# Optimization experiments

Measured on AMD Instinct MI355X. Metric: run time of the kernel, lower is better.

## Reference

```python
import jax, jax.numpy as jnp
import numpy as np

N_NODES = 50000
N_EDGES = 800000
D = 128
L = 3


def setup_inputs() -> dict:
    key = jax.random.key(0)
    k1, k2, k3 = jax.random.split(key, 3)
    x = jax.random.normal(k1, (N_NODES, D), dtype=jnp.float32)
    edge_index = jax.random.randint(k2, (2, N_EDGES), 0, N_NODES, dtype=jnp.int64)
    # per-layer GCNConv weights [L, in, out], bias [L, out] (zeros, as nn.Linear default bias is small),
    # PReLU per-channel slopes initialized to 0.25 (torch default)
    Ws = jax.random.normal(k3, (L, D, D), dtype=jnp.float32) / np.sqrt(D)
    bs = jnp.zeros((L, D), dtype=jnp.float32)
    alphas = jnp.full((L, D), 0.25, dtype=jnp.float32)
    return {"x": x, "edge_index": edge_index, "Ws": Ws, "bs": bs, "alphas": alphas}


def reference(x, edge_index, Ws, bs, alphas):
    N = x.shape[0]
    # PyG gcn_norm with edge_weight=None: unit weights, add self-loops (fill value 1),
    # symmetric normalization deg^{-1/2}[row] * deg^{-1/2}[col], aggregate at col (target).
    loop = jnp.arange(N, dtype=edge_index.dtype)
    row = jnp.concatenate([edge_index[0], loop])  # [E+N] source
    col = jnp.concatenate([edge_index[1], loop])  # [E+N] target
    deg = jax.ops.segment_sum(jnp.ones(row.shape[0], x.dtype), col, num_segments=N)
    dinv = jax.lax.rsqrt(deg)  # deg >= 1 due to self-loops
    norm = dinv[row] * dinv[col]  # [E+N]

    z = x
    for l in range(Ws.shape[0]):
        h = z @ Ws[l]  # linear transform [N, D]
        # gather -> scale -> scatter-add aggregation
        agg = jax.ops.segment_sum(h[row] * norm[:, None], col, num_segments=N)
        out = agg + bs[l]
        z = jnp.where(out >= 0, out, alphas[l] * out)  # per-channel PReLU
    return z
```

## Files before the change

### kernel.cpp

```cpp
#include <hip/hip_runtime.h>

#define N_NODES 50000
#define N_EDGES 800000
#define D 128
#define L 3
#define CAP 56

typedef __attribute__((ext_vector_type(8))) short short8;
typedef __attribute__((ext_vector_type(16))) float f32x16;

__device__ __forceinline__ unsigned int bf16_rne(float f) {
  unsigned int u = __float_as_uint(f);
  return (u + 0x7FFFu + ((u >> 16) & 1u)) >> 16;
}


__global__ __launch_bounds__(256) void zero_k(unsigned int* deg) {
  int i = blockIdx.x * 256 + threadIdx.x;
  if (i < N_NODES) deg[i] = 0u;
}

__global__ __launch_bounds__(256) void build_k(const int* __restrict__ rows,
                                               const int* __restrict__ cols,
                                               unsigned int* deg,
                                               unsigned int* __restrict__ csr) {
  int e = blockIdx.x * 256 + threadIdx.x;
  if (e >= N_EDGES) return;
  int c = cols[e];
  unsigned int r = atomicAdd(&deg[c], 1u);
  if (r < CAP) csr[(size_t)c * CAP + r] = (unsigned int)rows[e];
}

__global__ __launch_bounds__(256) void dinv_k(float* dinv_f, const unsigned int* deg) {
  int i = blockIdx.x * 256 + threadIdx.x;
  if (i < N_NODES) dinv_f[i] = rsqrtf((float)(deg[i] + 1u));
}

__global__ __launch_bounds__(256) void wconv_k(const float* __restrict__ Ws,
                                               unsigned int* __restrict__ Whi,
                                               unsigned int* __restrict__ Wlo) {
  int id = blockIdx.x * 256 + threadIdx.x;
  if (id >= L * 128 * 64) return;
  int kd = id & 63;
  int c = (id >> 6) & 127;
  int l = id >> 13;
  const float* W = Ws + (size_t)l * D * D;
  float w0 = W[(size_t)(2 * kd) * 128 + c];
  float w1 = W[(size_t)(2 * kd + 1) * 128 + c];
  unsigned int h0 = bf16_rne(w0), h1 = bf16_rne(w1);
  float f0 = __uint_as_float(h0 << 16), f1 = __uint_as_float(h1 << 16);
  unsigned int l0 = bf16_rne(w0 - f0), l1 = bf16_rne(w1 - f1);
  Whi[id] = h0 | (h1 << 16);
  Wlo[id] = l0 | (l1 << 16);
}

__global__ __launch_bounds__(256) void gather_k(const unsigned int* __restrict__ deg,
                                                const unsigned int* __restrict__ csr,
                                                const float* __restrict__ dinv,
                                                const float* __restrict__ Z,
                                                unsigned int* __restrict__ AGGhi,
                                                unsigned int* __restrict__ AGGlo) {
  int wid = (blockIdx.x * 256 + threadIdx.x) >> 6;
  int lane = threadIdx.x & 63;
  if (wid >= N_NODES) return;
  const float2* Z2 = (const float2*)Z;
  float di = dinv[wid];
  float2 z = Z2[(size_t)wid * 64 + lane];
  float sx = di * z.x, sy = di * z.y;
  unsigned int cnt = deg[wid];
  if (cnt > CAP) cnt = CAP;
  unsigned int s = 0u;
  float w = 0.f;
  if (lane < (int)cnt) {
    s = csr[(size_t)wid * CAP + lane];
    w = dinv[s];
  }
  unsigned int j = 0;
  for (; j + 8u <= cnt; j += 8u) {
    unsigned int ss[8];
    float wws[8];
#pragma unroll
    for (int t = 0; t < 8; ++t) {
      ss[t] = __shfl(s, (int)(j + t), 64);
      wws[t] = __shfl(w, (int)(j + t), 64);
    }
    float2 v[8];
#pragma unroll
    for (int t = 0; t < 8; ++t) v[t] = Z2[(size_t)ss[t] * 64 + lane];
#pragma unroll
    for (int t = 0; t < 8; ++t) {
      sx += wws[t] * v[t].x;
      sy += wws[t] * v[t].y;
    }
  }
  for (; j < cnt; ++j) {
    unsigned int s0 = __shfl(s, (int)j, 64);
    float w0 = __shfl(w, (int)j, 64);
    float2 v0 = Z2[(size_t)s0 * 64 + lane];
    sx += w0 * v0.x;
    sy += w0 * v0.y;
  }
  sx *= di;
  sy *= di;
  unsigned int hx = bf16_rne(sx), hy = bf16_rne(sy);
  float fx = __uint_as_float(hx << 16), fy = __uint_as_float(hy << 16);
  unsigned int lx = bf16_rne(sx - fx), ly = bf16_rne(sy - fy);
  AGGhi[(size_t)wid * 64 + lane] = hx | (hy << 16);
  AGGlo[(size_t)wid * 64 + lane] = lx | (ly << 16);
}

__global__ __launch_bounds__(64) void gemm_mfma_k(const unsigned int* __restrict__ Phi,
                                                  const unsigned int* __restrict__ Plo,
                                                  const unsigned int* __restrict__ Whi,
                                                  const unsigned int* __restrict__ Wlo,
                                                  const float* __restrict__ bias,
                                                  const float* __restrict__ alpha,
                                                  float* __restrict__ out) {
  const int lane = threadIdx.x;
  const int kg = lane >> 5;
  const int cl = lane & 31;
  const int rb = blockIdx.x * 32;
  const int row = rb + cl;
  const int ar = row < N_NODES ? row : N_NODES - 1;

  f32x16 acc[4];
#pragma unroll
  for (int cf = 0; cf < 4; ++cf)
#pragma unroll
    for (int j = 0; j < 16; ++j) acc[cf][j] = 0.f;

#pragma unroll
  for (int ks = 0; ks < 8; ++ks) {
    int pb = ks * 8 + kg * 4;
    short8 ahi = *(const short8*)&Phi[(size_t)ar * 64 + pb];
    short8 alo = *(const short8*)&Plo[(size_t)ar * 64 + pb];
#pragma unroll
    for (int cf = 0; cf < 4; ++cf) {
      int cc = cf * 32 + cl;
      short8 bhi = *(const short8*)&Whi[(size_t)cc * 64 + pb];
      short8 blo = *(const short8*)&Wlo[(size_t)cc * 64 + pb];
      acc[cf] = __builtin_amdgcn_mfma_f32_32x32x16_bf16(ahi, bhi, acc[cf], 0, 0, 0);
      acc[cf] = __builtin_amdgcn_mfma_f32_32x32x16_bf16(ahi, blo, acc[cf], 0, 0, 0);
      acc[cf] = __builtin_amdgcn_mfma_f32_32x32x16_bf16(alo, bhi, acc[cf], 0, 0, 0);
    }
  }

#pragma unroll
  for (int cf = 0; cf < 4; ++cf) {
    int col = cf * 32 + cl;
    float bl = bias[col], al = alpha[col];
#pragma unroll
    for (int j = 0; j < 16; ++j) {
      int r = rb + 4 * kg + (j & 3) + 8 * (j >> 2);
      if (r < N_NODES) {
        float v = acc[cf][j] + bl;
        out[(size_t)r * D + col] = v >= 0.f ? v : al * v;
      }
    }
  }
}


extern "C" void kernel_launch(void* const* d_in, const int* in_sizes, int n_in,
                              void* d_out, int out_size, void* d_ws, size_t ws_size,
                              hipStream_t stream) {
  const float* x      = (const float*)d_in[0];
  const int*   ei     = (const int*)d_in[1];
  const float* Ws     = (const float*)d_in[2];
  const float* bs     = (const float*)d_in[3];
  const float* alphas = (const float*)d_in[4];
  float* out = (float*)d_out;

  const int* rows = ei;
  const int* cols = ei + N_EDGES;

  char* ws = (char*)d_ws;
  const size_t NPAD = (((size_t)N_NODES * 4 + 255) / 256) * 256;
  const size_t CSRPAD = (((size_t)N_NODES * CAP * 4 + 255) / 256) * 256;
  const size_t AGGPAD = (((size_t)N_NODES * 64 * 4 + 255) / 256) * 256;
  const size_t WPAD = (((size_t)L * 128 * 64 * 4 + 255) / 256) * 256;
  float*        dinv  = (float*)ws;         ws += NPAD;
  unsigned int* deg   = (unsigned int*)ws;  ws += NPAD;
  unsigned int* csr   = (unsigned int*)ws;  ws += CSRPAD;
  unsigned int* AGGhi = (unsigned int*)ws;  ws += AGGPAD;
  unsigned int* AGGlo = (unsigned int*)ws;  ws += AGGPAD;
  unsigned int* Whi   = (unsigned int*)ws;  ws += WPAD;
  unsigned int* Wlo   = (unsigned int*)ws;  ws += WPAD;
  float* Z = out;

  zero_k<<<(N_NODES + 255) / 256, 256, 0, stream>>>(deg);
  build_k<<<(N_EDGES + 255) / 256, 256, 0, stream>>>(rows, cols, deg, csr);
  dinv_k<<<(N_NODES + 255) / 256, 256, 0, stream>>>(dinv, deg);
  wconv_k<<<(L * 128 * 64 + 255) / 256, 256, 0, stream>>>(Ws, Whi, Wlo);

  for (int l = 0; l < L; ++l) {
    const float* zin = (l == 0) ? x : Z;
    gather_k<<<(N_NODES * 64 + 255) / 256, 256, 0, stream>>>(deg, csr, dinv, zin, AGGhi, AGGlo);
    gemm_mfma_k<<<(N_NODES + 31) / 32, 64, 0, stream>>>(
        AGGhi, AGGlo, Whi + (size_t)l * 128 * 64, Wlo + (size_t)l * 128 * 64,
        bs + (size_t)l * D, alphas + (size_t)l * D, Z);
  }
}
```

Before: 318.2 us.

## Stage weights in LDS for 4-wave GEMM blocks and fold dinv into gather

The GEMM kernel now uses 256-thread blocks covering 128 rows. Each block stages the hi/lo bf16 weight halves into padded shared memory, in two K-halves, so all four waves share them instead of each wave reading W from global or L2. Separately, the dinv kernel and its buffer are removed, and the gather kernel computes rsqrt(deg+1) inline for the node and its neighbors. This saves one launch, at the cost of extra rsqrt work and deg lookups during gather.

```diff
diff --git a/kernel.cpp b/kernel.cpp
--- a/kernel.cpp
+++ b/kernel.cpp
@@ -29,11 +29,6 @@
   int c = cols[e];
   unsigned int r = atomicAdd(&deg[c], 1u);
   if (r < CAP) csr[(size_t)c * CAP + r] = (unsigned int)rows[e];
-}
-
-__global__ __launch_bounds__(256) void dinv_k(float* dinv_f, const unsigned int* deg) {
-  int i = blockIdx.x * 256 + threadIdx.x;
-  if (i < N_NODES) dinv_f[i] = rsqrtf((float)(deg[i] + 1u));
 }
 
 __global__ __launch_bounds__(256) void wconv_k(const float* __restrict__ Ws,
@@ -56,7 +51,6 @@
 
 __global__ __launch_bounds__(256) void gather_k(const unsigned int* __restrict__ deg,
                                                 const unsigned int* __restrict__ csr,
-                                                const float* __restrict__ dinv,
                                                 const float* __restrict__ Z,
                                                 unsigned int* __restrict__ AGGhi,
                                                 unsigned int* __restrict__ AGGlo) {
@@ -64,16 +58,16 @@
   int lane = threadIdx.x & 63;
   if (wid >= N_NODES) return;
   const float2* Z2 = (const float2*)Z;
-  float di = dinv[wid];
+  unsigned int dg = deg[wid];
+  float di = rsqrtf((float)(dg + 1u));
   float2 z = Z2[(size_t)wid * 64 + lane];
   float sx = di * z.x, sy = di * z.y;
-  unsigned int cnt = deg[wid];
-  if (cnt > CAP) cnt = CAP;
+  unsigned int cnt = dg > CAP ? CAP : dg;
   unsigned int s = 0u;
   float w = 0.f;
   if (lane < (int)cnt) {
     s = csr[(size_t)wid * CAP + lane];
-    w = dinv[s];
+    w = rsqrtf((float)(deg[s] + 1u));
   }
   unsigned int j = 0;
   for (; j + 8u <= cnt; j += 8u) {
@@ -109,18 +103,22 @@
   AGGlo[(size_t)wid * 64 + lane] = lx | (ly << 16);
 }
 
-__global__ __launch_bounds__(64) void gemm_mfma_k(const unsigned int* __restrict__ Phi,
-                                                  const unsigned int* __restrict__ Plo,
-                                                  const unsigned int* __restrict__ Whi,
-                                                  const unsigned int* __restrict__ Wlo,
-                                                  const float* __restrict__ bias,
-                                                  const float* __restrict__ alpha,
-                                                  float* __restrict__ out) {
-  const int lane = threadIdx.x;
+__global__ __launch_bounds__(256) void gemm_mfma_k(const unsigned int* __restrict__ Phi,
+                                                   const unsigned int* __restrict__ Plo,
+                                                   const unsigned int* __restrict__ Whi,
+                                                   const unsigned int* __restrict__ Wlo,
+                                                   const float* __restrict__ bias,
+                                                   const float* __restrict__ alpha,
+                                                   float* __restrict__ out) {
+  __shared__ unsigned int sWhi[128 * 36];
+  __shared__ unsigned int sWlo[128 * 36];
+  const int tid = threadIdx.x;
+  const int lane = tid & 63;
+  const int w = tid >> 6;
   const int kg = lane >> 5;
   const int cl = lane & 31;
-  const int rb = blockIdx.x * 32;
-  const int row = rb + cl;
+  const int rb = blockIdx.x * 128;
+  const int row = rb + w * 32 + cl;
   const int ar = row < N_NODES ? row : N_NODES - 1;
 
   f32x16 acc[4];
@@ -129,19 +127,33 @@
 #pragma unroll
     for (int j = 0; j < 16; ++j) acc[cf][j] = 0.f;
 
-#pragma unroll
-  for (int ks = 0; ks < 8; ++ks) {
-    int pb = ks * 8 + kg * 4;
-    short8 ahi = *(const short8*)&Phi[(size_t)ar * 64 + pb];
-    short8 alo = *(const short8*)&Plo[(size_t)ar * 64 + pb];
-#pragma unroll
-    for (int cf = 0; cf < 4; ++cf) {
-      int cc = cf * 32 + cl;
-      short8 bhi = *(const short8*)&Whi[(size_t)cc * 64 + pb];
-      short8 blo = *(const short8*)&Wlo[(size_t)cc * 64 + pb];
-      acc[cf] = __builtin_amdgcn_mfma_f32_32x32x16_bf16(ahi, bhi, acc[cf], 0, 0, 0);
-      acc[cf] = __builtin_amdgcn_mfma_f32_32x32x16_bf16(ahi, blo, acc[cf], 0, 0, 0);
-      acc[cf] = __builtin_amdgcn_mfma_f32_32x32x16_bf16(alo, bhi, acc[cf], 0, 0, 0);
+  for (int h = 0; h < 2; ++h) {
+    if (h) __syncthreads();
+#pragma unroll
+    for (int j = 0; j < 16; ++j) {
+      int id = j * 256 + tid;
+      int kd = id & 31;
+      int c = id >> 5;
+      sWhi[c * 36 + kd] = Whi[(size_t)c * 64 + h * 32 + kd];
+      sWlo[c * 36 + kd] = Wlo[(size_t)c * 64 + h * 32 + kd];
+    }
+    __syncthreads();
+
+#pragma unroll
+    for (int ks4 = 0; ks4 < 4; ++ks4) {
+      int pb = h * 32 + ks4 * 8 + kg * 4;
+      int lpb = ks4 * 8 + kg * 4;
+      short8 ahi = *(const short8*)&Phi[(size_t)ar * 64 + pb];
+      short8 alo = *(const short8*)&Plo[(size_t)ar * 64 + pb];
+#pragma unroll
+      for (int cf = 0; cf < 4; ++cf) {
+        int cc = cf * 32 + cl;
+        short8 bhi = *(const short8*)&sWhi[cc * 36 + lpb];
+        short8 blo = *(const short8*)&sWlo[cc * 36 + lpb];
+        acc[cf] = __builtin_amdgcn_mfma_f32_32x32x16_bf16(ahi, bhi, acc[cf], 0, 0, 0);
+        acc[cf] = __builtin_amdgcn_mfma_f32_32x32x16_bf16(ahi, blo, acc[cf], 0, 0, 0);
+        acc[cf] = __builtin_amdgcn_mfma_f32_32x32x16_bf16(alo, bhi, acc[cf], 0, 0, 0);
+      }
     }
   }
 
@@ -151,7 +163,7 @@
     float bl = bias[col], al = alpha[col];
 #pragma unroll
     for (int j = 0; j < 16; ++j) {
-      int r = rb + 4 * kg + (j & 3) + 8 * (j >> 2);
+      int r = rb + w * 32 + 4 * kg + (j & 3) + 8 * (j >> 2);
       if (r < N_NODES) {
         float v = acc[cf][j] + bl;
         out[(size_t)r * D + col] = v >= 0.f ? v : al * v;
@@ -179,7 +191,6 @@
   const size_t CSRPAD = (((size_t)N_NODES * CAP * 4 + 255) / 256) * 256;
   const size_t AGGPAD = (((size_t)N_NODES * 64 * 4 + 255) / 256) * 256;
   const size_t WPAD = (((size_t)L * 128 * 64 * 4 + 255) / 256) * 256;
-  float*        dinv  = (float*)ws;         ws += NPAD;
   unsigned int* deg   = (unsigned int*)ws;  ws += NPAD;
   unsigned int* csr   = (unsigned int*)ws;  ws += CSRPAD;
   unsigned int* AGGhi = (unsigned int*)ws;  ws += AGGPAD;
@@ -190,13 +201,12 @@
 
   zero_k<<<(N_NODES + 255) / 256, 256, 0, stream>>>(deg);
   build_k<<<(N_EDGES + 255) / 256, 256, 0, stream>>>(rows, cols, deg, csr);
-  dinv_k<<<(N_NODES + 255) / 256, 256, 0, stream>>>(dinv, deg);
   wconv_k<<<(L * 128 * 64 + 255) / 256, 256, 0, stream>>>(Ws, Whi, Wlo);
 
   for (int l = 0; l < L; ++l) {
     const float* zin = (l == 0) ? x : Z;
-    gather_k<<<(N_NODES * 64 + 255) / 256, 256, 0, stream>>>(deg, csr, dinv, zin, AGGhi, AGGlo);
-    gemm_mfma_k<<<(N_NODES + 31) / 32, 64, 0, stream>>>(
+    gather_k<<<(N_NODES * 64 + 255) / 256, 256, 0, stream>>>(deg, csr, zin, AGGhi, AGGlo);
+    gemm_mfma_k<<<(N_NODES + 127) / 128, 256, 0, stream>>>(
         AGGhi, AGGlo, Whi + (size_t)l * 128 * 64, Wlo + (size_t)l * 128 * 64,
         bs + (size_t)l * D, alphas + (size_t)l * D, Z);
   }
```

After: 305.2 us. 1.04x faster.
